# Performance work log

Hardware: AMD Instinct MI355X
Metric: run time of the kernel (lower is better)

## Reference

```python
import math
import jax, jax.numpy as jnp
import numpy as np

B, S, H = 4, 2048, 1024      # batch, seq_len, hidden_size
E, K, I = 8, 2, 1024         # n_routed_experts, top_k, expert intermediate
NSH = 2                      # n_shared_experts -> shared intermediate = NSH*I
CF, RSF = 1.25, 1.0          # capacity_factor, routed_scaling_factor


def setup_inputs() -> dict:
    key = jax.random.key(0)
    ks = jax.random.split(key, 8)
    w = lambda k, sh: jax.random.normal(k, sh, dtype=jnp.float32) * 0.02
    return {
        "hidden_states": jax.random.normal(ks[0], (B, S, H), dtype=jnp.float32),
        "gate_w":  w(ks[1], (E, H)),          # router weight (torch Linear layout)
        "we_gate": w(ks[2], (E, I, H)),       # per-expert gate_proj
        "we_up":   w(ks[3], (E, I, H)),       # per-expert up_proj
        "we_down": w(ks[4], (E, H, I)),       # per-expert down_proj
        "ws_gate": w(ks[5], (NSH * I, H)),    # shared expert gate_proj
        "ws_up":   w(ks[6], (NSH * I, H)),
        "ws_down": w(ks[7], (H, NSH * I)),
    }


def reference(hidden_states, gate_w, we_gate, we_up, we_down, ws_gate, ws_up, ws_down):
    orig_shape = hidden_states.shape
    x = hidden_states.reshape(-1, H)                       # [N, H]
    N = x.shape[0]

    # ---- gate (fp32 softmax + top-k, normalized, scaled) ----
    logits = x.astype(jnp.float32) @ gate_w.astype(jnp.float32).T   # [N, E]
    scores = jax.nn.softmax(logits, axis=-1)
    topk_w, topk_idx = jax.lax.top_k(scores, K)                      # [N, K]
    topk_w = topk_w / (topk_w.sum(-1, keepdims=True) + 1e-20) * RSF  # norm_topk_prob

    # ---- capacity masking: position of each (token,k) slot within its expert ----
    capacity = math.ceil(CF * N * K / E)
    flat = topk_idx.reshape(-1)                                      # [N*K]
    one_hot = jax.nn.one_hot(flat, E, dtype=jnp.int32)               # [N*K, E]
    pos = jnp.cumsum(one_hot, axis=0) - 1                            # running count per expert
    pos_tok = jnp.take_along_axis(pos, flat[:, None], axis=1)[:, 0]  # [N*K]
    keep = (pos_tok < capacity).reshape(N, K)
    topk_w = topk_w * keep.astype(topk_w.dtype)

    # ---- combine weights per (token, expert); dropped slots contribute 0 ----
    comb = jnp.zeros((N, E), jnp.float32).at[jnp.arange(N)[:, None], topk_idx].add(topk_w)

    # ---- routed experts: dense SwiGLU per expert, weighted combine ----
    g = jnp.einsum('nh,eih->nei', x, we_gate)                        # [N, E, I]
    u = jnp.einsum('nh,eih->nei', x, we_up)
    eo = jnp.einsum('nei,ehi->neh', jax.nn.silu(g) * u, we_down)     # [N, E, H]
    y = jnp.einsum('neh,ne->nh', eo, comb)                           # [N, H]

    # ---- shared experts ----
    sh = (jax.nn.silu(x @ ws_gate.T) * (x @ ws_up.T)) @ ws_down.T    # [N, H]

    return (y + sh).reshape(orig_shape)
```

## Files before the change

kernel.cpp:

```cpp
#include <hip/hip_runtime.h>

typedef unsigned short u16;

#define NTOK 8192
#define HD   1024
#define NEXP 8
#define CAP  2560

typedef __bf16 bf16x8 __attribute__((ext_vector_type(8)));
typedef float  f32x4  __attribute__((ext_vector_type(4)));

__device__ __forceinline__ u16 f2bf(float f){
  union { float f; unsigned u; } v; v.f = f;
  return (u16)((v.u + 0x7fffu + ((v.u >> 16) & 1u)) >> 16);
}
__device__ __forceinline__ float bf2f(u16 h){
  union { unsigned u; float f; } v; v.u = ((unsigned)h) << 16; return v.f;
}

__device__ __forceinline__ void async16(const void* g, void* l){
  __builtin_amdgcn_global_load_lds((__attribute__((address_space(1))) void*)(g),
                                   (__attribute__((address_space(3))) void*)(l), 16, 0, 0);
}

__global__ __launch_bounds__(256)
void prep_kernel(const float* __restrict__ x, const float* __restrict__ gate_w,
                 const float* __restrict__ we_gate, const float* __restrict__ we_up,
                 const float* __restrict__ we_down, const float* __restrict__ ws_gate,
                 const float* __restrict__ ws_up, const float* __restrict__ ws_down,
                 u16* __restrict__ x_bf, u16* __restrict__ wg_bf, u16* __restrict__ wu_bf,
                 u16* __restrict__ wd_bf, u16* __restrict__ wsg_bf, u16* __restrict__ wsu_bf,
                 u16* __restrict__ wsd_bf,
                 int* __restrict__ topk_idx, float* __restrict__ topk_w){
  __shared__ float gw[NEXP * HD];
  int bid = blockIdx.x;
  int t = threadIdx.x;
  if (bid < 2048){
    for (int i = t; i < NEXP * HD; i += 256) gw[i] = gate_w[i];
    __syncthreads();
    int wave = t >> 6, l = t & 63;
    int tok = bid * 4 + wave;
    const float* xr = x + (size_t)tok * HD;
    double acc[NEXP];
#pragma unroll
    for (int e = 0; e < NEXP; e++) acc[e] = 0.0;
    for (int j = 0; j < 16; j++){
      int h = j * 64 + l;
      double xv = (double)xr[h];
#pragma unroll
      for (int e = 0; e < NEXP; e++) acc[e] += xv * (double)gw[e * HD + h];
    }
#pragma unroll
    for (int e = 0; e < NEXP; e++){
      double v = acc[e];
#pragma unroll
      for (int off = 32; off > 0; off >>= 1) v += __shfl_down(v, off, 64);
      acc[e] = v;
    }
    if (l == 0){
      int i0 = 0; double l0 = acc[0];
#pragma unroll
      for (int e = 1; e < NEXP; e++) if (acc[e] > l0){ l0 = acc[e]; i0 = e; }
      int i1 = -1; double l1 = -1e300;
#pragma unroll
      for (int e = 0; e < NEXP; e++) if (e != i0 && acc[e] > l1){ l1 = acc[e]; i1 = e; }
      double e1 = exp(l1 - l0);
      double s  = 1.0 + e1;
      topk_idx[tok * 2 + 0] = i0;
      topk_idx[tok * 2 + 1] = i1;
      topk_w [tok * 2 + 0] = (float)(1.0 / s);
      topk_w [tok * 2 + 1] = (float)(e1 / s);
    }
  } else {
    long long g = (long long)(bid - 2048) * 256 + t;
    const float4* s; ushort4* d; long long off;
    if      (g <  2097152){ s = (const float4*)x;       d = (ushort4*)x_bf;   off = 0; }
    else if (g <  4194304){ s = (const float4*)we_gate; d = (ushort4*)wg_bf;  off = 2097152; }
    else if (g <  6291456){ s = (const float4*)we_up;   d = (ushort4*)wu_bf;  off = 4194304; }
    else if (g <  8388608){ s = (const float4*)we_down; d = (ushort4*)wd_bf;  off = 6291456; }
    else if (g <  8912896){ s = (const float4*)ws_gate; d = (ushort4*)wsg_bf; off = 8388608; }
    else if (g <  9437184){ s = (const float4*)ws_up;   d = (ushort4*)wsu_bf; off = 8912896; }
    else                  { s = (const float4*)ws_down; d = (ushort4*)wsd_bf; off = 9437184; }
    long long i = g - off;
    float4 v = s[i];
    ushort4 o;
    o.x = f2bf(v.x); o.y = f2bf(v.y); o.z = f2bf(v.z); o.w = f2bf(v.w);
    d[i] = o;
  }
}

__global__ __launch_bounds__(256)
void scan_p1(const int* __restrict__ topk_idx, int* __restrict__ chunk_hist){
  __shared__ int wcnt[4 * NEXP];
  int t = threadIdx.x, w = t >> 6, l = t & 63;
  int my_e = topk_idx[blockIdx.x * 256 + t];
#pragma unroll
  for (int e = 0; e < NEXP; e++){
    unsigned long long m = __ballot(my_e == e);
    if (l == e) wcnt[w * NEXP + e] = __popcll(m);
  }
  __syncthreads();
  if (t < NEXP){
    int s = 0;
#pragma unroll
    for (int w2 = 0; w2 < 4; w2++) s += wcnt[w2 * NEXP + t];
    chunk_hist[blockIdx.x * NEXP + t] = s;
  }
}

__global__ __launch_bounds__(256)
void scan_p2(const int* __restrict__ topk_idx, const float* __restrict__ topk_w,
             const int* __restrict__ chunk_hist,
             int* __restrict__ tok_list, float* __restrict__ w_list,
             int* __restrict__ slot_map, int* __restrict__ ne){
  __shared__ int hist_s[64 * NEXP];
  __shared__ int base_s[NEXP];
  __shared__ int wcnt[4 * NEXP];
  int t = threadIdx.x, w = t >> 6, l = t & 63;
  int chunk = blockIdx.x;
#pragma unroll
  for (int i = 0; i < 2; i++) hist_s[i * 256 + t] = chunk_hist[i * 256 + t];
  __syncthreads();
  if (t < NEXP){
    int b = 0, tot = 0;
    for (int c = 0; c < 64; c++){
      if (c == chunk) b = tot;
      tot += hist_s[c * NEXP + t];
    }
    base_s[t] = b;
    if (chunk == 0) ne[t] = tot < CAP ? tot : CAP;
  }
  int slot = chunk * 256 + t;
  int my_e = topk_idx[slot];
  float my_w = topk_w[slot];
  unsigned long long mymask = 0;
#pragma unroll
  for (int e = 0; e < NEXP; e++){
    unsigned long long m = __ballot(my_e == e);
    if (my_e == e) mymask = m;
    if (l == e) wcnt[w * NEXP + e] = __popcll(m);
  }
  __syncthreads();
  if (t < NEXP){
    int run = 0;
#pragma unroll
    for (int w2 = 0; w2 < 4; w2++){ int v = wcnt[w2 * NEXP + t]; wcnt[w2 * NEXP + t] = run; run += v; }
  }
  __syncthreads();
  int pos = base_s[my_e] + wcnt[w * NEXP + my_e] + __popcll(mymask & ((1ull << l) - 1ull));
  if (pos < CAP){
    tok_list[my_e * CAP + pos] = slot >> 1;
    w_list [my_e * CAP + pos] = my_w;
    slot_map[slot] = my_e * CAP + pos;
  } else {
    slot_map[slot] = -1;
  }
}

__global__ __launch_bounds__(256)
void gu_kernel(const u16* __restrict__ x_bf,
               const u16* __restrict__ wg, const u16* __restrict__ wu,
               const u16* __restrict__ wsg, const u16* __restrict__ wsu,
               u16* __restrict__ Hr, u16* __restrict__ Hs,
               const int* __restrict__ tok_list, const int* __restrict__ ne)
{
  __shared__ u16 As[128 * 64];
  __shared__ u16 Bs[128 * 64];

  const int bid = blockIdx.x;
  const bool routed = bid < 2560;
  int m0, n0, ldc, n_valid;
  const u16 *B0, *B1;
  u16* C;
  const int* tl = nullptr;
  if (routed){
    int e = bid & 7, r = bid >> 3;
    m0 = (r >> 4) * 128; n0 = (r & 15) * 64;
    B0 = wg + (size_t)e * (1024 * 1024);
    B1 = wu + (size_t)e * (1024 * 1024);
    C  = Hr + (size_t)e * (CAP * 1024);
    ldc = 1024;
    n_valid = ne[e];
    tl = tok_list + e * CAP;
    if (m0 >= n_valid) return;
  } else {
    int b2 = bid - 2560;
    n0 = (b2 / 64) * 64; m0 = (b2 % 64) * 128;
    B0 = wsg; B1 = wsu; C = Hs; ldc = 2048; n_valid = 1 << 30;
  }

  const int tid = threadIdx.x;
  const int wv  = tid >> 6;
  const int l   = tid & 63;
  const int lr  = l >> 3;
  const int cb  = (l & 7) ^ lr;

  const u16* aptr[4];
  const u16* bptr[4];
#pragma unroll
  for (int i = 0; i < 4; i++){
    int chunk = i * 4 + wv;
    int arow  = m0 + chunk * 8 + lr;
    if (routed){
      int r2 = arow < n_valid ? arow : (n_valid - 1);
      aptr[i] = x_bf + (size_t)tl[r2] * 1024 + cb * 8;
    } else {
      aptr[i] = x_bf + (size_t)arow * 1024 + cb * 8;
    }
    int rn = chunk * 8 + lr;
    int w  = rn >> 6;
    int jq = (rn >> 4) & 3;
    int rl = rn & 15;
    int icol = n0 + w * 32 + (jq & 1) * 16 + rl;
    bptr[i] = ((jq < 2) ? B0 : B1) + (size_t)icol * 1024 + cb * 8;
  }

  const int wm = wv & 1, wn = wv >> 1;
  const int col = l & 15, quad = l >> 4;
  const int rr = col & 7, ch = col >> 3;

  f32x4 acc[4][4];
#pragma unroll
  for (int i = 0; i < 4; i++)
#pragma unroll
    for (int j = 0; j < 4; j++)
      acc[i][j] = (f32x4){0.f, 0.f, 0.f, 0.f};

  for (int k0 = 0; k0 < 1024; k0 += 64){
#pragma unroll
    for (int i = 0; i < 4; i++){
      int chunk = i * 4 + wv;
      async16(aptr[i] + k0, &As[chunk * 512 + l * 8]);
      async16(bptr[i] + k0, &Bs[chunk * 512 + l * 8]);
    }
    __syncthreads();
#pragma unroll
    for (int s = 0; s < 2; s++){
      const int so = (rr * 8 + ((quad + s * 4) ^ rr)) * 8;
      bf16x8 a[4], b[4];
#pragma unroll
      for (int i = 0; i < 4; i++) a[i] = *(const bf16x8*)&As[(wm * 8 + i * 2 + ch) * 512 + so];
#pragma unroll
      for (int j = 0; j < 4; j++) b[j] = *(const bf16x8*)&Bs[(wn * 8 + j * 2 + ch) * 512 + so];
#pragma unroll
      for (int i = 0; i < 4; i++)
#pragma unroll
        for (int j = 0; j < 4; j++)
          acc[i][j] = __builtin_amdgcn_mfma_f32_16x16x32_bf16(a[i], b[j], acc[i][j], 0, 0, 0);
    }
    __syncthreads();
  }

#pragma unroll
  for (int i = 0; i < 4; i++)
#pragma unroll
    for (int r = 0; r < 4; r++){
      int row = m0 + wm * 64 + i * 16 + quad * 4 + r;
#pragma unroll
      for (int j = 0; j < 2; j++){
        int cg = n0 + wn * 32 + j * 16 + col;
        float g = acc[i][j][r], u = acc[i][j + 2][r];
        float h = (g / (1.f + __expf(-g))) * u;
        C[(size_t)row * ldc + cg] = f2bf(h);
      }
    }
}

__global__ __launch_bounds__(256)
void down_kernel(const u16* __restrict__ Hr, const u16* __restrict__ wd,
                 const u16* __restrict__ Hs, const u16* __restrict__ wsd,
                 u16* __restrict__ Ebuf, float* __restrict__ out,
                 const float* __restrict__ w_list, const int* __restrict__ ne)
{
  __shared__ u16 As[128 * 64];
  __shared__ u16 Bs[128 * 64];

  const int bid = blockIdx.x;
  const bool routed = bid < 1280;
  int m0, n0, n_valid, K, e = 0;
  const u16 *Ab, *Bb;
  if (routed){
    e = bid & 7; int r = bid >> 3;
    m0 = (r >> 3) * 128; n0 = (r & 7) * 128;
    Ab = Hr + (size_t)e * (CAP * 1024);
    Bb = wd + (size_t)e * (1024 * 1024);
    K = 1024;
    n_valid = ne[e];
    if (m0 >= n_valid) return;
  } else {
    int b2 = bid - 1280;
    n0 = (b2 & 7) * 128; m0 = (b2 >> 3) * 128;
    Ab = Hs; Bb = wsd; K = 2048; n_valid = 1 << 30;
  }

  const int tid = threadIdx.x;
  const int wv  = tid >> 6;
  const int l   = tid & 63;
  const int lr  = l >> 3;
  const int cb  = (l & 7) ^ lr;

  const u16* aptr[4];
  const u16* bptr[4];
#pragma unroll
  for (int i = 0; i < 4; i++){
    int chunk = i * 4 + wv;
    aptr[i] = Ab + (size_t)(m0 + chunk * 8 + lr) * K + cb * 8;
    bptr[i] = Bb + (size_t)(n0 + chunk * 8 + lr) * K + cb * 8;
  }

  const int wm = wv & 1, wn = wv >> 1;
  const int col = l & 15, quad = l >> 4;
  const int rr = col & 7, ch = col >> 3;

  f32x4 acc[4][4];
#pragma unroll
  for (int i = 0; i < 4; i++)
#pragma unroll
    for (int j = 0; j < 4; j++)
      acc[i][j] = (f32x4){0.f, 0.f, 0.f, 0.f};

  for (int k0 = 0; k0 < K; k0 += 64){
#pragma unroll
    for (int i = 0; i < 4; i++){
      int chunk = i * 4 + wv;
      async16(aptr[i] + k0, &As[chunk * 512 + l * 8]);
      async16(bptr[i] + k0, &Bs[chunk * 512 + l * 8]);
    }
    __syncthreads();
#pragma unroll
    for (int s = 0; s < 2; s++){
      const int so = (rr * 8 + ((quad + s * 4) ^ rr)) * 8;
      bf16x8 a[4], b[4];
#pragma unroll
      for (int i = 0; i < 4; i++) a[i] = *(const bf16x8*)&As[(wm * 8 + i * 2 + ch) * 512 + so];
#pragma unroll
      for (int j = 0; j < 4; j++) b[j] = *(const bf16x8*)&Bs[(wn * 8 + j * 2 + ch) * 512 + so];
#pragma unroll
      for (int i = 0; i < 4; i++)
#pragma unroll
        for (int j = 0; j < 4; j++)
          acc[i][j] = __builtin_amdgcn_mfma_f32_16x16x32_bf16(a[i], b[j], acc[i][j], 0, 0, 0);
    }
    __syncthreads();
  }

  if (routed){
    u16* C = Ebuf + (size_t)e * (CAP * 1024);
    const float* wl = w_list + e * CAP;
#pragma unroll
    for (int i = 0; i < 4; i++)
#pragma unroll
      for (int r = 0; r < 4; r++){
        int row = m0 + wm * 64 + i * 16 + quad * 4 + r;
        if (row < n_valid){
          float wgt = wl[row];
#pragma unroll
          for (int j = 0; j < 4; j++){
            int cg = n0 + wn * 64 + j * 16 + col;
            C[(size_t)row * 1024 + cg] = f2bf(wgt * acc[i][j][r]);
          }
        }
      }
  } else {
#pragma unroll
    for (int i = 0; i < 4; i++)
#pragma unroll
      for (int r = 0; r < 4; r++){
        int row = m0 + wm * 64 + i * 16 + quad * 4 + r;
#pragma unroll
        for (int j = 0; j < 4; j++){
          int cg = n0 + wn * 64 + j * 16 + col;
          out[(size_t)row * 1024 + cg] = acc[i][j][r];
        }
      }
  }
}

__global__ __launch_bounds__(256)
void combine_kernel(float* __restrict__ out, const u16* __restrict__ Ebuf,
                    const int* __restrict__ slot_map){
  long long g = (long long)blockIdx.x * 256 + threadIdx.x;
  int row = (int)(g >> 8);
  int c4  = (int)(g & 255);
  int s0 = slot_map[row * 2 + 0];
  int s1 = slot_map[row * 2 + 1];
  float4 v = ((float4*)out)[g];
  if (s0 >= 0){
    ushort4 a = ((const ushort4*)Ebuf)[(size_t)s0 * 256 + c4];
    v.x += bf2f(a.x); v.y += bf2f(a.y); v.z += bf2f(a.z); v.w += bf2f(a.w);
  }
  if (s1 >= 0){
    ushort4 a = ((const ushort4*)Ebuf)[(size_t)s1 * 256 + c4];
    v.x += bf2f(a.x); v.y += bf2f(a.y); v.z += bf2f(a.z); v.w += bf2f(a.w);
  }
  ((float4*)out)[g] = v;
}

extern "C" void kernel_launch(void* const* d_in, const int* in_sizes, int n_in,
                              void* d_out, int out_size, void* d_ws, size_t ws_size,
                              hipStream_t stream){
  const float* x       = (const float*)d_in[0];
  const float* gate_w  = (const float*)d_in[1];
  const float* we_gate = (const float*)d_in[2];
  const float* we_up   = (const float*)d_in[3];
  const float* we_down = (const float*)d_in[4];
  const float* ws_gate = (const float*)d_in[5];
  const float* ws_up   = (const float*)d_in[6];
  const float* ws_down = (const float*)d_in[7];
  float* out = (float*)d_out;

  char* p = (char*)d_ws;
  u16* x_bf   = (u16*)p; p += (size_t)NTOK * HD * 2;
  u16* wg_bf  = (u16*)p; p += (size_t)NEXP * 1024 * 1024 * 2;
  u16* wu_bf  = (u16*)p; p += (size_t)NEXP * 1024 * 1024 * 2;
  u16* wsg_bf = (u16*)p; p += (size_t)2048 * 1024 * 2;
  u16* wsu_bf = (u16*)p; p += (size_t)2048 * 1024 * 2;
  u16* wd_bf  = (u16*)p; p += (size_t)NEXP * 1024 * 1024 * 2;
  u16* wsd_bf = (u16*)p; p += (size_t)1024 * 2048 * 2;
  u16* Hr     = (u16*)p; p += (size_t)NEXP * CAP * 1024 * 2;
  u16* Hs     = (u16*)p; p += (size_t)NTOK * 2048 * 2;
  int*   topk_idx   = (int*)p;   p += (size_t)NTOK * 2 * 4;
  float* topk_w     = (float*)p; p += (size_t)NTOK * 2 * 4;
  int*   tok_list   = (int*)p;   p += (size_t)NEXP * CAP * 4;
  float* w_list     = (float*)p; p += (size_t)NEXP * CAP * 4;
  int*   slot_map   = (int*)p;   p += (size_t)NTOK * 2 * 4;
  int*   chunk_hist = (int*)p;   p += 64 * NEXP * 4;
  int*   ne         = (int*)p;   p += 128;
  u16* Ebuf = wg_bf;

  prep_kernel<<<dim3(40960), dim3(256), 0, stream>>>(
      x, gate_w, we_gate, we_up, we_down, ws_gate, ws_up, ws_down,
      x_bf, wg_bf, wu_bf, wd_bf, wsg_bf, wsu_bf, wsd_bf, topk_idx, topk_w);

  scan_p1<<<dim3(64), dim3(256), 0, stream>>>(topk_idx, chunk_hist);
  scan_p2<<<dim3(64), dim3(256), 0, stream>>>(topk_idx, topk_w, chunk_hist,
                                              tok_list, w_list, slot_map, ne);

  gu_kernel<<<dim3(4608), dim3(256), 0, stream>>>(
      x_bf, wg_bf, wu_bf, wsg_bf, wsu_bf, Hr, Hs, tok_list, ne);

  down_kernel<<<dim3(1792), dim3(256), 0, stream>>>(
      Hr, wd_bf, Hs, wsd_bf, Ebuf, out, w_list, ne);

  combine_kernel<<<dim3(8192), dim3(256), 0, stream>>>(out, Ebuf, slot_map);
}
```

Baseline: 486.5 us.

## Fuse x conversion and histogram into router, interleave down tiles, batch combine

The router pass now writes the bf16 copy of x while reading it and accumulates the per-chunk expert histogram with atomics, which removes the scan_p1 launch and a second read of x. A memset zeroes the histogram first. The down kernel interleaves routed and shared tiles in a 5:2 pattern to balance work across the grid. The combine kernel processes four float4 elements per thread with a quarter of the blocks. Atomics add contention in exchange for one fewer launch.

```diff
diff --git a/kernel.cpp b/kernel.cpp
--- a/kernel.cpp
+++ b/kernel.cpp
@@ -31,7 +31,8 @@
                  u16* __restrict__ x_bf, u16* __restrict__ wg_bf, u16* __restrict__ wu_bf,
                  u16* __restrict__ wd_bf, u16* __restrict__ wsg_bf, u16* __restrict__ wsu_bf,
                  u16* __restrict__ wsd_bf,
-                 int* __restrict__ topk_idx, float* __restrict__ topk_w){
+                 int* __restrict__ topk_idx, float* __restrict__ topk_w,
+                 int* __restrict__ chunk_hist){
   __shared__ float gw[NEXP * HD];
   int bid = blockIdx.x;
   int t = threadIdx.x;
@@ -41,12 +42,15 @@
     int wave = t >> 6, l = t & 63;
     int tok = bid * 4 + wave;
     const float* xr = x + (size_t)tok * HD;
+    u16* xbr = x_bf + (size_t)tok * HD;
     double acc[NEXP];
 #pragma unroll
     for (int e = 0; e < NEXP; e++) acc[e] = 0.0;
     for (int j = 0; j < 16; j++){
       int h = j * 64 + l;
-      double xv = (double)xr[h];
+      float xf = xr[h];
+      xbr[h] = f2bf(xf);
+      double xv = (double)xf;
 #pragma unroll
       for (int e = 0; e < NEXP; e++) acc[e] += xv * (double)gw[e * HD + h];
     }
@@ -70,41 +74,24 @@
       topk_idx[tok * 2 + 1] = i1;
       topk_w [tok * 2 + 0] = (float)(1.0 / s);
       topk_w [tok * 2 + 1] = (float)(e1 / s);
+      int chunk = tok >> 7;
+      atomicAdd(&chunk_hist[chunk * NEXP + i0], 1);
+      atomicAdd(&chunk_hist[chunk * NEXP + i1], 1);
     }
   } else {
     long long g = (long long)(bid - 2048) * 256 + t;
     const float4* s; ushort4* d; long long off;
-    if      (g <  2097152){ s = (const float4*)x;       d = (ushort4*)x_bf;   off = 0; }
-    else if (g <  4194304){ s = (const float4*)we_gate; d = (ushort4*)wg_bf;  off = 2097152; }
-    else if (g <  6291456){ s = (const float4*)we_up;   d = (ushort4*)wu_bf;  off = 4194304; }
-    else if (g <  8388608){ s = (const float4*)we_down; d = (ushort4*)wd_bf;  off = 6291456; }
-    else if (g <  8912896){ s = (const float4*)ws_gate; d = (ushort4*)wsg_bf; off = 8388608; }
-    else if (g <  9437184){ s = (const float4*)ws_up;   d = (ushort4*)wsu_bf; off = 8912896; }
-    else                  { s = (const float4*)ws_down; d = (ushort4*)wsd_bf; off = 9437184; }
+    if      (g <  2097152){ s = (const float4*)we_gate; d = (ushort4*)wg_bf;  off = 0; }
+    else if (g <  4194304){ s = (const float4*)we_up;   d = (ushort4*)wu_bf;  off = 2097152; }
+    else if (g <  6291456){ s = (const float4*)we_down; d = (ushort4*)wd_bf;  off = 4194304; }
+    else if (g <  6815744){ s = (const float4*)ws_gate; d = (ushort4*)wsg_bf; off = 6291456; }
+    else if (g <  7340032){ s = (const float4*)ws_up;   d = (ushort4*)wsu_bf; off = 6815744; }
+    else                  { s = (const float4*)ws_down; d = (ushort4*)wsd_bf; off = 7340032; }
     long long i = g - off;
     float4 v = s[i];
     ushort4 o;
     o.x = f2bf(v.x); o.y = f2bf(v.y); o.z = f2bf(v.z); o.w = f2bf(v.w);
     d[i] = o;
-  }
-}
-
-__global__ __launch_bounds__(256)
-void scan_p1(const int* __restrict__ topk_idx, int* __restrict__ chunk_hist){
-  __shared__ int wcnt[4 * NEXP];
-  int t = threadIdx.x, w = t >> 6, l = t & 63;
-  int my_e = topk_idx[blockIdx.x * 256 + t];
-#pragma unroll
-  for (int e = 0; e < NEXP; e++){
-    unsigned long long m = __ballot(my_e == e);
-    if (l == e) wcnt[w * NEXP + e] = __popcll(m);
-  }
-  __syncthreads();
-  if (t < NEXP){
-    int s = 0;
-#pragma unroll
-    for (int w2 = 0; w2 < 4; w2++) s += wcnt[w2 * NEXP + t];
-    chunk_hist[blockIdx.x * NEXP + t] = s;
   }
 }
 
@@ -276,11 +263,13 @@
   __shared__ u16 Bs[128 * 64];
 
   const int bid = blockIdx.x;
-  const bool routed = bid < 1280;
+  const int m7 = bid % 7, d7 = bid / 7;
+  const bool routed = m7 < 5;
   int m0, n0, n_valid, K, e = 0;
   const u16 *Ab, *Bb;
   if (routed){
-    e = bid & 7; int r = bid >> 3;
+    int rid = d7 * 5 + m7;
+    e = rid & 7; int r = rid >> 3;
     m0 = (r >> 3) * 128; n0 = (r & 7) * 128;
     Ab = Hr + (size_t)e * (CAP * 1024);
     Bb = wd + (size_t)e * (1024 * 1024);
@@ -288,8 +277,8 @@
     n_valid = ne[e];
     if (m0 >= n_valid) return;
   } else {
-    int b2 = bid - 1280;
-    n0 = (b2 & 7) * 128; m0 = (b2 >> 3) * 128;
+    int sid = d7 * 2 + (m7 - 5);
+    n0 = (sid & 7) * 128; m0 = (sid >> 3) * 128;
     Ab = Hs; Bb = wsd; K = 2048; n_valid = 1 << 30;
   }
 
@@ -379,21 +368,25 @@
 __global__ __launch_bounds__(256)
 void combine_kernel(float* __restrict__ out, const u16* __restrict__ Ebuf,
                     const int* __restrict__ slot_map){
-  long long g = (long long)blockIdx.x * 256 + threadIdx.x;
-  int row = (int)(g >> 8);
-  int c4  = (int)(g & 255);
-  int s0 = slot_map[row * 2 + 0];
-  int s1 = slot_map[row * 2 + 1];
-  float4 v = ((float4*)out)[g];
-  if (s0 >= 0){
-    ushort4 a = ((const ushort4*)Ebuf)[(size_t)s0 * 256 + c4];
-    v.x += bf2f(a.x); v.y += bf2f(a.y); v.z += bf2f(a.z); v.w += bf2f(a.w);
-  }
-  if (s1 >= 0){
-    ushort4 a = ((const ushort4*)Ebuf)[(size_t)s1 * 256 + c4];
-    v.x += bf2f(a.x); v.y += bf2f(a.y); v.z += bf2f(a.z); v.w += bf2f(a.w);
-  }
-  ((float4*)out)[g] = v;
+  long long g0 = (long long)blockIdx.x * 256 + threadIdx.x;
+#pragma unroll
+  for (int k = 0; k < 4; k++){
+    long long g = g0 + (long long)k * 524288;
+    int row = (int)(g >> 8);
+    int c4  = (int)(g & 255);
+    int s0 = slot_map[row * 2 + 0];
+    int s1 = slot_map[row * 2 + 1];
+    float4 v = ((float4*)out)[g];
+    if (s0 >= 0){
+      ushort4 a = ((const ushort4*)Ebuf)[(size_t)s0 * 256 + c4];
+      v.x += bf2f(a.x); v.y += bf2f(a.y); v.z += bf2f(a.z); v.w += bf2f(a.w);
+    }
+    if (s1 >= 0){
+      ushort4 a = ((const ushort4*)Ebuf)[(size_t)s1 * 256 + c4];
+      v.x += bf2f(a.x); v.y += bf2f(a.y); v.z += bf2f(a.z); v.w += bf2f(a.w);
+    }
+    ((float4*)out)[g] = v;
+  }
 }
 
 extern "C" void kernel_launch(void* const* d_in, const int* in_sizes, int n_in,
@@ -428,11 +421,12 @@
   int*   ne         = (int*)p;   p += 128;
   u16* Ebuf = wg_bf;
 
-  prep_kernel<<<dim3(40960), dim3(256), 0, stream>>>(
+  hipMemsetAsync(chunk_hist, 0, 64 * NEXP * 4, stream);
+
+  prep_kernel<<<dim3(32768), dim3(256), 0, stream>>>(
       x, gate_w, we_gate, we_up, we_down, ws_gate, ws_up, ws_down,
-      x_bf, wg_bf, wu_bf, wd_bf, wsg_bf, wsu_bf, wsd_bf, topk_idx, topk_w);
-
-  scan_p1<<<dim3(64), dim3(256), 0, stream>>>(topk_idx, chunk_hist);
+      x_bf, wg_bf, wu_bf, wd_bf, wsg_bf, wsu_bf, wsd_bf, topk_idx, topk_w, chunk_hist);
+
   scan_p2<<<dim3(64), dim3(256), 0, stream>>>(topk_idx, topk_w, chunk_hist,
                                               tok_list, w_list, slot_map, ne);
 
@@ -442,5 +436,5 @@
   down_kernel<<<dim3(1792), dim3(256), 0, stream>>>(
       Hr, wd_bf, Hs, wsd_bf, Ebuf, out, w_list, ne);
 
-  combine_kernel<<<dim3(8192), dim3(256), 0, stream>>>(out, Ebuf, slot_map);
-}
+  combine_kernel<<<dim3(2048), dim3(256), 0, stream>>>(out, Ebuf, slot_map);
+}
```

Measured after the change: 514.8 us. +5.8%, slower.
